# Performance work log

Hardware: AMD Instinct MI355X
Metric: run time of the kernel (lower is better)

The kernel has to match this reference:

```python
import jax, jax.numpy as jnp
import numpy as np

B, C, H, W = 64, 256, 64, 64
RATIO, K = 16, 8
PLANES = C // 2          # context_modeling hidden = int(in_planes*0.5)
HIDDEN = C // RATIO      # net hidden
ATT_CH = K // 2          # kernel-attention hidden
TEMP = 30.0
EPS = 1e-5


def setup_inputs() -> dict:
    key = jax.random.key(0)
    ks = jax.random.split(key, 16)
    s = lambda k, shape: jax.random.normal(k, shape, dtype=jnp.float32) * 0.05
    return {
        "x": jax.random.normal(ks[0], (B, C, H, W), dtype=jnp.float32),
        # conv_mask: Conv2d(C,1,1) with bias
        "w_mask": s(ks[1], (1, C)), "b_mask": jnp.zeros((1,), jnp.float32),
        # context_modeling: Conv2d(C,PLANES,1)+bias, LayerNorm([PLANES,1,1]), GELU, Conv2d(PLANES,C,1)+bias
        "w_cm1": s(ks[2], (PLANES, C)), "b_cm1": jnp.zeros((PLANES,), jnp.float32),
        "ln_w": jnp.ones((PLANES,), jnp.float32), "ln_b": jnp.zeros((PLANES,), jnp.float32),
        "w_cm2": s(ks[3], (C, PLANES)), "b_cm2": jnp.zeros((C,), jnp.float32),
        # net: Conv2d(C,HIDDEN,1,bias=False), ReLU, Conv2d(HIDDEN,K,1,bias=False)
        "w_net1": s(ks[4], (HIDDEN, C)), "w_net2": s(ks[5], (K, HIDDEN)),
        # kernel attention branch (K != 1)
        "w_fc": s(ks[6], (ATT_CH, K)),
        "bn_w": jnp.ones((ATT_CH,), jnp.float32), "bn_b": jnp.zeros((ATT_CH,), jnp.float32),
        "bn_mean": jnp.zeros((ATT_CH,), jnp.float32), "bn_var": jnp.ones((ATT_CH,), jnp.float32),
        "w_kfc": s(ks[7], (K, ATT_CH)),
    }


def reference(x, w_mask, b_mask, w_cm1, b_cm1, ln_w, ln_b, w_cm2, b_cm2,
              w_net1, w_net2, w_fc, bn_w, bn_b, bn_mean, bn_var, w_kfc):
    b, c, h, w = x.shape
    # beta_c: global average pool -> [B, C]
    beta_c = jnp.mean(x, axis=(2, 3))
    # global_pool: softmax(conv_mask(x)) over HW, spatially weighted sum of x
    mask = jnp.einsum('bchw,oc->bohw', x, w_mask)[:, 0] + b_mask[0]      # [B,H,W]
    mask = jax.nn.softmax(mask.reshape(b, h * w), axis=-1)               # softmax over HW
    context = jnp.einsum('bchw,bs->bc', x, mask.reshape(b, h, w).reshape(b, -1).reshape(b, h * w)) if False else \
        jnp.einsum('bcs,bs->bc', x.reshape(b, c, h * w), mask)           # [B,C]
    # context_modeling: 1x1 conv -> LayerNorm over channels -> GELU -> 1x1 conv
    t = context @ w_cm1.T + b_cm1                                        # [B, PLANES]
    mu = jnp.mean(t, axis=-1, keepdims=True)
    var = jnp.mean((t - mu) ** 2, axis=-1, keepdims=True)
    t = (t - mu) * jax.lax.rsqrt(var + EPS) * ln_w + ln_b
    t = jax.nn.gelu(t, approximate=False)
    beta_g = t @ w_cm2.T + b_cm2                                         # [B, C]
    # beta_s: channel-mean/max maps, tiled [avg,max,avg,max,...], spatial mean
    a = jnp.mean(jnp.mean(x, axis=1), axis=(1, 2))                       # [B]
    m = jnp.mean(jnp.max(x, axis=1), axis=(1, 2))                        # [B]
    beta_s = jnp.tile(jnp.stack([a, m], axis=-1), (1, c // 2))           # [B, C]
    out = beta_c + beta_g + beta_s                                       # [B, C]
    # net: conv1x1 -> ReLU -> conv1x1
    out = jax.nn.relu(out @ w_net1.T) @ w_net2.T                         # [B, K]
    # dynamic kernel attention (eval-mode BatchNorm on 1x1 spatial)
    ka = out @ w_fc.T                                                    # [B, K/2]
    ka = (ka - bn_mean) * jax.lax.rsqrt(bn_var + EPS) * bn_w + bn_b
    kernel = jax.nn.sigmoid(jax.nn.relu(ka) @ w_kfc.T)                   # [B, K]
    out = out * kernel
    return jax.nn.softmax(out / TEMP, axis=-1)                           # [B, K]
```

## Files before the change

kernel.cpp:

```cpp
#include <hip/hip_runtime.h>
#include <math.h>

#define BB   64
#define CC   256
#define HWQ  4096
#define TILE 64
#define ITER 4
#define QB   16
#define NBLK (BB * QB)
#define TPB  256

#define WS_BETA 0
#define WS_CTX  (NBLK * CC)
#define WS_Z    (2 * NBLK * CC)
#define WS_M    (WS_Z + NBLK)

__global__ __launch_bounds__(TPB, 4) void pass1(
    const float* __restrict__ x,
    const float* __restrict__ w_mask,
    const float* __restrict__ b_mask,
    float* __restrict__ ws)
{
    __shared__ __align__(16) float wm[CC];
    __shared__ __align__(16) float redL[16 * 64];
    __shared__ __align__(16) float redM[16 * 64];
    __shared__ __align__(16) float tileP[TILE];
    __shared__ float scr[CC * 17];

    const int tid = threadIdx.x;
    const int b   = blockIdx.x >> 4;
    const int q   = blockIdx.x & 15;
    const int hi  = tid >> 4;
    const int j   = tid & 15;
    const float* xb = x + (size_t)b * CC * HWQ + q * (TILE * ITER);

    wm[tid] = w_mask[tid];
    __syncthreads();
    const float bm = b_mask[0];

    float smP[16], cxP[16];
    #pragma unroll
    for (int i = 0; i < 16; ++i) { smP[i] = 0.f; cxP[i] = 0.f; }
    float zTot = 0.f, mTot = 0.f;

    for (int it = 0; it < ITER; ++it) {
        float4 cur[16];
        #pragma unroll
        for (int i = 0; i < 16; ++i) {
            const int c = i * 16 + hi;
            cur[i] = *reinterpret_cast<const float4*>(
                xb + (size_t)c * HWQ + it * TILE + 4 * j);
        }

        float lp0 = 0.f, lp1 = 0.f, lp2 = 0.f, lp3 = 0.f;
        float mp0 = -3.4e38f, mp1 = -3.4e38f, mp2 = -3.4e38f, mp3 = -3.4e38f;
        #pragma unroll
        for (int i = 0; i < 16; ++i) {
            const float w = wm[i * 16 + hi];
            const float4 v = cur[i];
            lp0 = fmaf(w, v.x, lp0); lp1 = fmaf(w, v.y, lp1);
            lp2 = fmaf(w, v.z, lp2); lp3 = fmaf(w, v.w, lp3);
            mp0 = fmaxf(mp0, v.x); mp1 = fmaxf(mp1, v.y);
            mp2 = fmaxf(mp2, v.z); mp3 = fmaxf(mp3, v.w);
        }
        reinterpret_cast<float4*>(redL)[tid] = make_float4(lp0, lp1, lp2, lp3);
        reinterpret_cast<float4*>(redM)[tid] = make_float4(mp0, mp1, mp2, mp3);
        __syncthreads();

        if (tid < TILE) {
            float lg = 0.f;
            #pragma unroll
            for (int h = 0; h < 16; ++h) lg += redL[h * 64 + tid];
            const float p = expf(lg + bm);
            tileP[tid] = p;
            float zs = p;
            #pragma unroll
            for (int off = 32; off > 0; off >>= 1) zs += __shfl_down(zs, off, 64);
            if (tid == 0) zTot += zs;
        } else if (tid < 2 * TILE) {
            const int s = tid - TILE;
            float cm = -3.4e38f;
            #pragma unroll
            for (int h = 0; h < 16; ++h) cm = fmaxf(cm, redM[h * 64 + s]);
            float cs = cm;
            #pragma unroll
            for (int off = 32; off > 0; off >>= 1) cs += __shfl_down(cs, off, 64);
            if (tid == TILE) mTot += cs;
        }
        __syncthreads();

        const float4 pv = reinterpret_cast<const float4*>(tileP)[j];
        #pragma unroll
        for (int i = 0; i < 16; ++i) {
            const float4 v = cur[i];
            smP[i] += (v.x + v.y) + (v.z + v.w);
            cxP[i] = fmaf(v.x, pv.x, fmaf(v.y, pv.y,
                     fmaf(v.z, pv.z, fmaf(v.w, pv.w, cxP[i]))));
        }
    }

    #pragma unroll
    for (int i = 0; i < 16; ++i) scr[(i * 16 + hi) * 17 + j] = smP[i];
    __syncthreads();
    {
        float sm = 0.f;
        #pragma unroll
        for (int k = 0; k < 16; ++k) sm += scr[tid * 17 + k];
        ws[WS_BETA + blockIdx.x * CC + tid] = sm;
    }
    __syncthreads();
    #pragma unroll
    for (int i = 0; i < 16; ++i) scr[(i * 16 + hi) * 17 + j] = cxP[i];
    __syncthreads();
    {
        float cx = 0.f;
        #pragma unroll
        for (int k = 0; k < 16; ++k) cx += scr[tid * 17 + k];
        ws[WS_CTX + blockIdx.x * CC + tid] = cx;
    }
    if (tid == 0)    ws[WS_Z + blockIdx.x] = zTot;
    if (tid == TILE) ws[WS_M + blockIdx.x] = mTot;
}

__global__ __launch_bounds__(TPB) void finalize(
    const float* __restrict__ ws,
    const float* __restrict__ w_cm1,  const float* __restrict__ b_cm1,
    const float* __restrict__ ln_w,   const float* __restrict__ ln_b,
    const float* __restrict__ w_cm2,  const float* __restrict__ b_cm2,
    const float* __restrict__ w_net1, const float* __restrict__ w_net2,
    const float* __restrict__ w_fc,   const float* __restrict__ bn_w,
    const float* __restrict__ bn_b,   const float* __restrict__ bn_mean,
    const float* __restrict__ bn_var, const float* __restrict__ w_kfc,
    float* __restrict__ out)
{
    __shared__ __align__(16) float s_beta[CC];
    __shared__ __align__(16) float s_ctx[CC];
    __shared__ __align__(16) float s_t[128];
    __shared__ __align__(16) float s_out[CC];
    __shared__ float s_h[16];
    __shared__ float s_o2[8];
    __shared__ float s_red[4];
    __shared__ float s_scal[4];
    __shared__ float s_zm[2];

    const int b = blockIdx.x, tid = threadIdx.x;

    float bc_s = 0.f, cx_s = 0.f;
    #pragma unroll
    for (int qq = 0; qq < QB; ++qq) {
        bc_s += ws[WS_BETA + (b * QB + qq) * CC + tid];
        cx_s += ws[WS_CTX  + (b * QB + qq) * CC + tid];
    }
    if (tid < 32) {
        float v = (tid < 16) ? ws[WS_Z + b * QB + tid]
                             : ws[WS_M + b * QB + (tid - 16)];
        v += __shfl_down(v, 8, 64);
        v += __shfl_down(v, 4, 64);
        v += __shfl_down(v, 2, 64);
        v += __shfl_down(v, 1, 64);
        if (tid == 0)  s_zm[0] = v;
        if (tid == 16) s_zm[1] = v;
    }
    __syncthreads();

    const float bc = bc_s * (1.f / 4096.f);
    const float cx = cx_s / s_zm[0];
    s_beta[tid] = bc;
    s_ctx[tid]  = cx;

    float av = bc;
    #pragma unroll
    for (int off = 32; off > 0; off >>= 1) av += __shfl_down(av, off, 64);
    if ((tid & 63) == 0) s_red[tid >> 6] = av;
    __syncthreads();
    if (tid == 0) {
        s_scal[0] = (s_red[0] + s_red[1] + s_red[2] + s_red[3]) * (1.f / 256.f);
        s_scal[1] = s_zm[1] * (1.f / 4096.f);
    }
    __syncthreads();

    if (tid < 128) {
        const float4* wr = reinterpret_cast<const float4*>(w_cm1 + tid * 256);
        const float4* cr = reinterpret_cast<const float4*>(s_ctx);
        float acc = 0.f;
        #pragma unroll 4
        for (int i = 0; i < 64; ++i) {
            const float4 w = wr[i], c4 = cr[i];
            acc = fmaf(w.x, c4.x, acc); acc = fmaf(w.y, c4.y, acc);
            acc = fmaf(w.z, c4.z, acc); acc = fmaf(w.w, c4.w, acc);
        }
        s_t[tid] = acc + b_cm1[tid];
    }
    __syncthreads();

    if (tid < 64) {
        float v = s_t[tid] + s_t[tid + 64];
        #pragma unroll
        for (int off = 32; off > 0; off >>= 1) v += __shfl_down(v, off, 64);
        float mu = __shfl(v, 0, 64) * (1.f / 128.f);
        const float d0 = s_t[tid] - mu, d1 = s_t[tid + 64] - mu;
        float vv = d0 * d0 + d1 * d1;
        #pragma unroll
        for (int off = 32; off > 0; off >>= 1) vv += __shfl_down(vv, off, 64);
        if (tid == 0) {
            s_scal[2] = mu;
            s_scal[3] = rsqrtf(vv * (1.f / 128.f) + 1e-5f);
        }
    }
    __syncthreads();

    if (tid < 128) {
        float g = (s_t[tid] - s_scal[2]) * s_scal[3] * ln_w[tid] + ln_b[tid];
        g = 0.5f * g * (1.0f + erff(g * 0.70710678118654752f));
        s_t[tid] = g;
    }
    __syncthreads();

    {
        const float4* wr = reinterpret_cast<const float4*>(w_cm2 + tid * 128);
        const float4* gr = reinterpret_cast<const float4*>(s_t);
        float acc = 0.f;
        #pragma unroll 4
        for (int i = 0; i < 32; ++i) {
            const float4 w = wr[i], g = gr[i];
            acc = fmaf(w.x, g.x, acc); acc = fmaf(w.y, g.y, acc);
            acc = fmaf(w.z, g.z, acc); acc = fmaf(w.w, g.w, acc);
        }
        const float bs = (tid & 1) ? s_scal[1] : s_scal[0];
        s_out[tid] = s_beta[tid] + acc + b_cm2[tid] + bs;
    }
    __syncthreads();

    if (tid < 16) {
        const float4* wr = reinterpret_cast<const float4*>(w_net1 + tid * 256);
        const float4* orr = reinterpret_cast<const float4*>(s_out);
        float acc = 0.f;
        #pragma unroll 4
        for (int i = 0; i < 64; ++i) {
            const float4 w = wr[i], o = orr[i];
            acc = fmaf(w.x, o.x, acc); acc = fmaf(w.y, o.y, acc);
            acc = fmaf(w.z, o.z, acc); acc = fmaf(w.w, o.w, acc);
        }
        s_h[tid] = fmaxf(acc, 0.f);
    }
    __syncthreads();

    if (tid < 8) {
        float acc = 0.f;
        #pragma unroll
        for (int jj = 0; jj < 16; ++jj) acc += s_h[jj] * w_net2[tid * 16 + jj];
        s_o2[tid] = acc;
    }
    __syncthreads();

    if (tid == 0) {
        float r[4];
        #pragma unroll
        for (int p = 0; p < 4; ++p) {
            float acc = 0.f;
            #pragma unroll
            for (int k = 0; k < 8; ++k) acc += s_o2[k] * w_fc[p * 8 + k];
            acc = (acc - bn_mean[p]) * rsqrtf(bn_var[p] + 1e-5f) * bn_w[p] + bn_b[p];
            r[p] = fmaxf(acc, 0.f);
        }
        float v[8], vmax = -3.4e38f;
        #pragma unroll
        for (int k = 0; k < 8; ++k) {
            float acc = 0.f;
            #pragma unroll
            for (int p = 0; p < 4; ++p) acc += r[p] * w_kfc[k * 4 + p];
            const float kr = 1.f / (1.f + expf(-acc));
            v[k] = s_o2[k] * kr * (1.f / 30.f);
            vmax = fmaxf(vmax, v[k]);
        }
        float zs = 0.f;
        #pragma unroll
        for (int k = 0; k < 8; ++k) { v[k] = expf(v[k] - vmax); zs += v[k]; }
        const float inv = 1.f / zs;
        #pragma unroll
        for (int k = 0; k < 8; ++k) out[b * 8 + k] = v[k] * inv;
    }
}

extern "C" void kernel_launch(void* const* d_in, const int* in_sizes, int n_in,
                              void* d_out, int out_size, void* d_ws, size_t ws_size,
                              hipStream_t stream) {
    const float* x       = (const float*)d_in[0];
    const float* w_mask  = (const float*)d_in[1];
    const float* b_mask  = (const float*)d_in[2];
    const float* w_cm1   = (const float*)d_in[3];
    const float* b_cm1   = (const float*)d_in[4];
    const float* ln_w    = (const float*)d_in[5];
    const float* ln_b    = (const float*)d_in[6];
    const float* w_cm2   = (const float*)d_in[7];
    const float* b_cm2   = (const float*)d_in[8];
    const float* w_net1  = (const float*)d_in[9];
    const float* w_net2  = (const float*)d_in[10];
    const float* w_fc    = (const float*)d_in[11];
    const float* bn_w    = (const float*)d_in[12];
    const float* bn_b    = (const float*)d_in[13];
    const float* bn_mean = (const float*)d_in[14];
    const float* bn_var  = (const float*)d_in[15];
    const float* w_kfc   = (const float*)d_in[16];
    float* out = (float*)d_out;
    float* ws  = (float*)d_ws;

    pass1<<<NBLK, TPB, 0, stream>>>(x, w_mask, b_mask, ws);
    finalize<<<BB, TPB, 0, stream>>>(ws, w_cm1, b_cm1, ln_w, ln_b, w_cm2, b_cm2,
                                     w_net1, w_net2, w_fc, bn_w, bn_b, bn_mean,
                                     bn_var, w_kfc, out);
}
```

Baseline: 420.2 us.

## Replace per-tile LDS reductions with wave shuffles and enlarge per-block work

Pass1 now gives each wave its own run of pixels, with the 16 channel groups spread across lanes. Mask logits and channel maxima are reduced with xor-shuffles instead of LDS buffers and two block barriers per tile. Mask weights move into registers, and the grid shrinks to 8 blocks per batch with double the iterations. Finalize now reduces 8 partials per batch instead of 16. In exchange, each channel row is read in shorter 64-byte contiguous segments, and occupancy is lower with fewer, heavier blocks.

Result: slower. 429.1 us (+2.1%).

```diff
diff --git a/kernel.cpp b/kernel.cpp
--- a/kernel.cpp
+++ b/kernel.cpp
@@ -4,9 +4,8 @@
 #define BB   64
 #define CC   256
 #define HWQ  4096
-#define TILE 64
-#define ITER 4
-#define QB   16
+#define ITER 8
+#define QB   8
 #define NBLK (BB * QB)
 #define TPB  256
 
@@ -15,27 +14,30 @@
 #define WS_Z    (2 * NBLK * CC)
 #define WS_M    (WS_Z + NBLK)
 
-__global__ __launch_bounds__(TPB, 4) void pass1(
+__global__ __launch_bounds__(TPB, 2) void pass1(
     const float* __restrict__ x,
     const float* __restrict__ w_mask,
     const float* __restrict__ b_mask,
     float* __restrict__ ws)
 {
     __shared__ __align__(16) float wm[CC];
-    __shared__ __align__(16) float redL[16 * 64];
-    __shared__ __align__(16) float redM[16 * 64];
-    __shared__ __align__(16) float tileP[TILE];
     __shared__ float scr[CC * 17];
-
-    const int tid = threadIdx.x;
-    const int b   = blockIdx.x >> 4;
-    const int q   = blockIdx.x & 15;
-    const int hi  = tid >> 4;
-    const int j   = tid & 15;
-    const float* xb = x + (size_t)b * CC * HWQ + q * (TILE * ITER);
+    __shared__ float s_z[4], s_m[4];
+
+    const int tid  = threadIdx.x;
+    const int w    = tid >> 6;
+    const int lane = tid & 63;
+    const int pg   = lane >> 4;
+    const int g    = lane & 15;
+    const int b    = blockIdx.x >> 3;
+    const int qw   = (blockIdx.x & 7) * 4 + w;
+    const float* xb = x + (size_t)b * CC * HWQ;
 
     wm[tid] = w_mask[tid];
     __syncthreads();
+    float wmr[16];
+    #pragma unroll
+    for (int i = 0; i < 16; ++i) wmr[i] = wm[i * 16 + g];
     const float bm = b_mask[0];
 
     float smP[16], cxP[16];
@@ -44,63 +46,68 @@
     float zTot = 0.f, mTot = 0.f;
 
     for (int it = 0; it < ITER; ++it) {
+        const int px0 = qw * 128 + it * 16 + pg * 4;
+
         float4 cur[16];
         #pragma unroll
         for (int i = 0; i < 16; ++i) {
-            const int c = i * 16 + hi;
             cur[i] = *reinterpret_cast<const float4*>(
-                xb + (size_t)c * HWQ + it * TILE + 4 * j);
-        }
-
-        float lp0 = 0.f, lp1 = 0.f, lp2 = 0.f, lp3 = 0.f;
-        float mp0 = -3.4e38f, mp1 = -3.4e38f, mp2 = -3.4e38f, mp3 = -3.4e38f;
+                xb + (size_t)(i * 16 + g) * HWQ + px0);
+        }
+
+        float lgx = 0.f, lgy = 0.f, lgz = 0.f, lgw = 0.f;
+        float mpx = -3.4e38f, mpy = -3.4e38f, mpz = -3.4e38f, mpw = -3.4e38f;
         #pragma unroll
         for (int i = 0; i < 16; ++i) {
-            const float w = wm[i * 16 + hi];
+            const float wv = wmr[i];
             const float4 v = cur[i];
-            lp0 = fmaf(w, v.x, lp0); lp1 = fmaf(w, v.y, lp1);
-            lp2 = fmaf(w, v.z, lp2); lp3 = fmaf(w, v.w, lp3);
-            mp0 = fmaxf(mp0, v.x); mp1 = fmaxf(mp1, v.y);
-            mp2 = fmaxf(mp2, v.z); mp3 = fmaxf(mp3, v.w);
-        }
-        reinterpret_cast<float4*>(redL)[tid] = make_float4(lp0, lp1, lp2, lp3);
-        reinterpret_cast<float4*>(redM)[tid] = make_float4(mp0, mp1, mp2, mp3);
-        __syncthreads();
-
-        if (tid < TILE) {
-            float lg = 0.f;
-            #pragma unroll
-            for (int h = 0; h < 16; ++h) lg += redL[h * 64 + tid];
-            const float p = expf(lg + bm);
-            tileP[tid] = p;
-            float zs = p;
-            #pragma unroll
-            for (int off = 32; off > 0; off >>= 1) zs += __shfl_down(zs, off, 64);
-            if (tid == 0) zTot += zs;
-        } else if (tid < 2 * TILE) {
-            const int s = tid - TILE;
-            float cm = -3.4e38f;
-            #pragma unroll
-            for (int h = 0; h < 16; ++h) cm = fmaxf(cm, redM[h * 64 + s]);
-            float cs = cm;
-            #pragma unroll
-            for (int off = 32; off > 0; off >>= 1) cs += __shfl_down(cs, off, 64);
-            if (tid == TILE) mTot += cs;
-        }
-        __syncthreads();
-
-        const float4 pv = reinterpret_cast<const float4*>(tileP)[j];
+            lgx = fmaf(wv, v.x, lgx); lgy = fmaf(wv, v.y, lgy);
+            lgz = fmaf(wv, v.z, lgz); lgw = fmaf(wv, v.w, lgw);
+            mpx = fmaxf(mpx, v.x); mpy = fmaxf(mpy, v.y);
+            mpz = fmaxf(mpz, v.z); mpw = fmaxf(mpw, v.w);
+        }
+
+        #pragma unroll
+        for (int mk = 1; mk < 16; mk <<= 1) {
+            lgx += __shfl_xor(lgx, mk, 64);
+            lgy += __shfl_xor(lgy, mk, 64);
+            lgz += __shfl_xor(lgz, mk, 64);
+            lgw += __shfl_xor(lgw, mk, 64);
+            mpx = fmaxf(mpx, __shfl_xor(mpx, mk, 64));
+            mpy = fmaxf(mpy, __shfl_xor(mpy, mk, 64));
+            mpz = fmaxf(mpz, __shfl_xor(mpz, mk, 64));
+            mpw = fmaxf(mpw, __shfl_xor(mpw, mk, 64));
+        }
+
+        float4 p;
+        p.x = expf(lgx + bm); p.y = expf(lgy + bm);
+        p.z = expf(lgz + bm); p.w = expf(lgw + bm);
+        if (g == 0) {
+            zTot += (p.x + p.y) + (p.z + p.w);
+            mTot += (mpx + mpy) + (mpz + mpw);
+        }
+
         #pragma unroll
         for (int i = 0; i < 16; ++i) {
             const float4 v = cur[i];
             smP[i] += (v.x + v.y) + (v.z + v.w);
-            cxP[i] = fmaf(v.x, pv.x, fmaf(v.y, pv.y,
-                     fmaf(v.z, pv.z, fmaf(v.w, pv.w, cxP[i]))));
-        }
-    }
-
-    #pragma unroll
-    for (int i = 0; i < 16; ++i) scr[(i * 16 + hi) * 17 + j] = smP[i];
+            cxP[i] = fmaf(v.x, p.x, fmaf(v.y, p.y,
+                     fmaf(v.z, p.z, fmaf(v.w, p.w, cxP[i]))));
+        }
+    }
+
+    {
+        float zs = zTot, ms = mTot;
+        #pragma unroll
+        for (int off = 32; off > 0; off >>= 1) {
+            zs += __shfl_down(zs, off, 64);
+            ms += __shfl_down(ms, off, 64);
+        }
+        if (lane == 0) { s_z[w] = zs; s_m[w] = ms; }
+    }
+
+    #pragma unroll
+    for (int i = 0; i < 16; ++i) scr[(i * 16 + g) * 17 + (tid >> 4)] = smP[i];
     __syncthreads();
     {
         float sm = 0.f;
@@ -110,7 +117,7 @@
     }
     __syncthreads();
     #pragma unroll
-    for (int i = 0; i < 16; ++i) scr[(i * 16 + hi) * 17 + j] = cxP[i];
+    for (int i = 0; i < 16; ++i) scr[(i * 16 + g) * 17 + (tid >> 4)] = cxP[i];
     __syncthreads();
     {
         float cx = 0.f;
@@ -118,8 +125,10 @@
         for (int k = 0; k < 16; ++k) cx += scr[tid * 17 + k];
         ws[WS_CTX + blockIdx.x * CC + tid] = cx;
     }
-    if (tid == 0)    ws[WS_Z + blockIdx.x] = zTot;
-    if (tid == TILE) ws[WS_M + blockIdx.x] = mTot;
+    if (tid == 0) {
+        ws[WS_Z + blockIdx.x] = (s_z[0] + s_z[1]) + (s_z[2] + s_z[3]);
+        ws[WS_M + blockIdx.x] = (s_m[0] + s_m[1]) + (s_m[2] + s_m[3]);
+    }
 }
 
 __global__ __launch_bounds__(TPB) void finalize(
@@ -151,15 +160,13 @@
         bc_s += ws[WS_BETA + (b * QB + qq) * CC + tid];
         cx_s += ws[WS_CTX  + (b * QB + qq) * CC + tid];
     }
-    if (tid < 32) {
-        float v = (tid < 16) ? ws[WS_Z + b * QB + tid]
-                             : ws[WS_M + b * QB + (tid - 16)];
-        v += __shfl_down(v, 8, 64);
+    if (tid < 16) {
+        float v = (tid < 8) ? ws[WS_Z + b * QB + tid] : ws[WS_M + b * QB + (tid - 8)];
         v += __shfl_down(v, 4, 64);
         v += __shfl_down(v, 2, 64);
         v += __shfl_down(v, 1, 64);
-        if (tid == 0)  s_zm[0] = v;
-        if (tid == 16) s_zm[1] = v;
+        if (tid == 0) s_zm[0] = v;
+        if (tid == 8) s_zm[1] = v;
     }
     __syncthreads();
 
```
